# Optimization experiments

Measured on AMD Instinct MI355X. Metric: run time of the kernel, lower is better.

Reference implementation:

```python
import jax, jax.numpy as jnp
import numpy as np

N = 8192       # batch size
BIT = 32       # hash code length
NCLASS = 100   # number of classes
ALPHA = 0.1    # config['alpha'] (quantization weight)
BEITA = 1.0    # config['beita'] (classification weight)
GAMMA = 0.1    # config['gamma'] (balancing weight)
P = 2          # config['p']


def setup_inputs() -> dict:
    key = jax.random.key(0)
    k1, k2, k3 = jax.random.split(key, 3)
    u = jax.random.normal(k1, (N, BIT), dtype=jnp.float32)
    Y = jax.random.normal(k2, (N, NCLASS), dtype=jnp.float32)
    labels = jax.random.randint(k3, (N,), 0, NCLASS)
    y = jax.nn.one_hot(labels, NCLASS, dtype=jnp.float32)  # one-hot targets
    return {"u": u, "Y": Y, "y": y}


def _hash_loss(u, y):
    n = u.shape[0]
    theta = (u @ u.T) * 0.5                       # [N, N]
    sim = (y @ y.T > 0).astype(u.dtype)           # [N, N] pairwise same-class
    # log(1 + exp(theta)) - Sim * theta  (logaddexp = stable same math)
    pair = jnp.logaddexp(0.0, theta) - sim * theta
    mask_pos = sim > 0
    s1 = sim.sum() - n                            # positives minus diagonal
    s0 = n * n - sim.sum()                        # negatives
    s0 = jnp.where(s0 == 0, 1.0, s0)
    s1 = jnp.where(s1 == 0, 1.0, s1)
    s = s0 + s1
    scale = jnp.where(mask_pos, s / s1, s / s0)
    pair = pair * scale
    # original subtracts diag of the *detached* rescaled matrix
    pair = pair - jax.lax.stop_gradient(jnp.diag(jnp.diag(pair)))
    count = n * (n - 1) / 2
    return pair.sum() / 2.0 / count


def reference(u, Y, y):
    likelihood_loss = _hash_loss(u, y)
    # CrossEntropyLoss with soft (one-hot float) targets
    logp = jax.nn.log_softmax(Y, axis=-1)
    classification_loss = -(y * logp).sum(axis=-1).mean()
    m = u.mean(axis=1)
    if P == 1:
        quantization_loss = ALPHA * jnp.abs(m).mean()
    else:
        quantization_loss = ALPHA * (m ** 2).mean()
    b = jnp.sign(u)
    balancing_loss = GAMMA * ((u - b) ** 2).mean()
    return likelihood_loss + BEITA * classification_loss + quantization_loss + balancing_loss
```

## Files before the change

### kernel.cpp

```cpp
#include <hip/hip_runtime.h>
#include <math.h>
#include <type_traits>

#define N 8192
#define BIT 32
#define NCLASS 100
#define ALPHA 0.1
#define BEITA 1.0
#define GAMMA 0.1

#define BT 128
#define NT (N / BT)
#define NPAIRBLK (NT * (NT + 1) / 2)
#define NPREP (N / 8)

typedef __attribute__((ext_vector_type(8))) short s16x8;
typedef __attribute__((ext_vector_type(4))) float f32x4;

static __device__ __forceinline__ unsigned short f2bf(float f) {
    unsigned int x = __float_as_uint(f);
    x += 0x7fff + ((x >> 16) & 1);
    return (unsigned short)(x >> 16);
}


__global__ __launch_bounds__(256) void prep_kernel(
    const float* __restrict__ u, const float* __restrict__ Y, const float* __restrict__ y,
    int* __restrict__ labels, double* __restrict__ Pc, double* __restrict__ Pm,
    double* __restrict__ Pb)
{
    const int t = threadIdx.x;
    const int lane = t & 63;
    const int w = t >> 6;
    const int row0 = blockIdx.x * 8;

    float wcls = 0.f;
    #pragma unroll
    for (int rr = 0; rr < 2; ++rr) {
        const int r = row0 + w * 2 + rr;
        const float* Yp = Y + (size_t)r * NCLASS;
        const float* yp = y + (size_t)r * NCLASS;
        const bool has2 = lane < (NCLASS - 64);
        float Y0 = Yp[lane];
        float Y1 = has2 ? Yp[64 + lane] : -1e30f;
        float y0 = yp[lane];
        float y1 = has2 ? yp[64 + lane] : 0.f;
        float m = fmaxf(Y0, Y1);
        #pragma unroll
        for (int o = 32; o; o >>= 1) m = fmaxf(m, __shfl_xor(m, o, 64));
        float e  = __expf(Y0 - m) + (has2 ? __expf(Y1 - m) : 0.f);
        float tg = y0 * Y0 + (has2 ? y1 * Y1 : 0.f);
        #pragma unroll
        for (int o = 32; o; o >>= 1) { e += __shfl_xor(e, o, 64); tg += __shfl_xor(tg, o, 64); }
        unsigned long long b0 = __ballot(y0 > 0.5f);
        unsigned long long b1 = __ballot(has2 && (y1 > 0.5f));
        if (lane == 0) {
            int lbl = b0 ? (__ffsll((long long)b0) - 1) : (64 + __ffsll((long long)b1) - 1);
            labels[r] = lbl;
            wcls += m + __logf(e) - tg;
        }
    }

    const float x = u[(size_t)row0 * BIT + t];
    float bb = (x > 0.f) ? 1.f : ((x < 0.f) ? -1.f : 0.f);
    float d = x - bb;
    float bal = d * d;
    float rs = x;
    #pragma unroll
    for (int o = 1; o < 32; o <<= 1) rs += __shfl_xor(rs, o, 64);
    float mrow = rs * (1.f / BIT);
    float m2 = ((t & 31) == 0) ? mrow * mrow : 0.f;
    #pragma unroll
    for (int o = 32; o; o >>= 1) { m2 += __shfl_down(m2, o, 64); bal += __shfl_down(bal, o, 64); }

    __shared__ double red[4][3];
    if (lane == 0) { red[w][0] = (double)wcls; red[w][1] = (double)m2; red[w][2] = (double)bal; }
    __syncthreads();
    if (t == 0) {
        Pc[blockIdx.x] = red[0][0] + red[1][0] + red[2][0] + red[3][0];
        Pm[blockIdx.x] = red[0][1] + red[1][1] + red[2][1] + red[3][1];
        Pb[blockIdx.x] = red[0][2] + red[1][2] + red[2][2] + red[3][2];
    }
}

__global__ __launch_bounds__(256, 4) void pair_kernel(
    const float* __restrict__ u, const int* __restrict__ labels,
    double* __restrict__ Ppos, double* __restrict__ Pneg)
{
    const int b = blockIdx.x;
    int ti = (int)(((float)(2 * NT + 1) - sqrtf((float)((2 * NT + 1) * (2 * NT + 1) - 8 * b))) * 0.5f);
    int S = ti * (2 * NT - ti + 1) / 2;
    if (S > b) { --ti; S = ti * (2 * NT - ti + 1) / 2; }
    else { int S2 = (ti + 1) * (2 * NT - ti) / 2; if (S2 <= b) { ++ti; S = S2; } }
    const int tj = ti + (b - S);
    const int i0 = ti * BT, j0 = tj * BT;

    __shared__ __align__(16) unsigned short Us[4][256][8];
    __shared__ int Ls[256];
    __shared__ float wredp[4], wredn[4];

    const int t = threadIdx.x;

    {
        const int g = (t < BT) ? (i0 + t) : (j0 + t - BT);
        const float4* p = (const float4*)(u + (size_t)g * BIT);
        #pragma unroll
        for (int c = 0; c < 4; ++c) {
            float4 v0 = p[2 * c], v1 = p[2 * c + 1];
            s16x8 fr;
            fr[0] = (short)f2bf(v0.x); fr[1] = (short)f2bf(v0.y);
            fr[2] = (short)f2bf(v0.z); fr[3] = (short)f2bf(v0.w);
            fr[4] = (short)f2bf(v1.x); fr[5] = (short)f2bf(v1.y);
            fr[6] = (short)f2bf(v1.z); fr[7] = (short)f2bf(v1.w);
            *(s16x8*)&Us[c][t][0] = fr;
        }
        Ls[t] = labels[g];
    }
    __syncthreads();

    const int lane = t & 63;
    const int w = t >> 6;
    const int wy = w >> 1, wx = w & 1;
    const int quad = lane >> 4, lr = lane & 15;

    s16x8 av[4], bv[4];
    #pragma unroll
    for (int x = 0; x < 4; ++x) {
        av[x] = *(const s16x8*)&Us[quad][wy * 64 + x * 16 + lr][0];
        bv[x] = *(const s16x8*)&Us[quad][128 + wx * 64 + x * 16 + lr][0];
    }
    int lbv[4], lav[16];
    #pragma unroll
    for (int c = 0; c < 4; ++c) lbv[c] = Ls[128 + wx * 64 + c * 16 + lr];
    #pragma unroll
    for (int a = 0; a < 4; ++a)
        #pragma unroll
        for (int r = 0; r < 4; ++r) lav[a * 4 + r] = Ls[wy * 64 + a * 16 + quad * 4 + r];

    float sp0 = 0.f, sp1 = 0.f, sn0 = 0.f, sn1 = 0.f;
    auto run = [&](auto DIAGC) {
        constexpr bool DIAG = decltype(DIAGC)::value;
        f32x4 accf[4][4];
        #pragma unroll
        for (int a = 0; a < 4; ++a)
            #pragma unroll
            for (int c = 0; c < 4; ++c)
                accf[a][c] = __builtin_amdgcn_mfma_f32_16x16x32_bf16(
                    av[a], bv[c], (f32x4){0.f, 0.f, 0.f, 0.f}, 0, 0, 0);

        #pragma unroll
        for (int a = 0; a < 4; ++a) {
            #pragma unroll
            for (int c = 0; c < 4; ++c) {
                const int lb = lbv[c];
                #pragma unroll
                for (int r = 0; r < 4; ++r) {
                    const float v = accf[a][c][r];
                    const bool sim = (lav[a * 4 + r] == lb);
                    float hv = 0.5f * v;
                    float e  = exp2f(-1.44269504f * fabsf(hv));
                    float lt = 0.69314718f * __log2f(1.f + e);
                    float tp = fmaxf(-hv, 0.f) + lt;
                    float tn = tp + hv;
                    if (DIAG) {
                        const int lrow = wy * 64 + a * 16 + quad * 4 + r;
                        const int lcol = wx * 64 + c * 16 + lr;
                        const bool keep = lcol > lrow;
                        tp = keep ? tp : 0.f;
                        tn = keep ? tn : 0.f;
                    }
                    float up = sim ? tp : 0.f;
                    float un = sim ? 0.f : tn;
                    if (r & 1) { sp1 += up; sn1 += un; }
                    else       { sp0 += up; sn0 += un; }
                }
            }
        }
    };
    if (ti == tj) run(std::integral_constant<bool, true>{});
    else          run(std::integral_constant<bool, false>{});

    float sp = sp0 + sp1, sn = sn0 + sn1;
    #pragma unroll
    for (int o = 32; o; o >>= 1) { sp += __shfl_down(sp, o, 64); sn += __shfl_down(sn, o, 64); }
    if (lane == 0) { wredp[w] = sp; wredn[w] = sn; }
    __syncthreads();
    if (t == 0) {
        Ppos[b] = (double)(wredp[0] + wredp[1] + wredp[2] + wredp[3]);
        Pneg[b] = (double)(wredn[0] + wredn[1] + wredn[2] + wredn[3]);
    }
}

__global__ __launch_bounds__(256) void fin_kernel(
    const int* __restrict__ labels, const double* __restrict__ Ppos,
    const double* __restrict__ Pneg, const double* __restrict__ Pc,
    const double* __restrict__ Pm, const double* __restrict__ Pb, float* __restrict__ out)
{
    __shared__ int h[128];
    __shared__ double red[4][5];
    __shared__ double scd[2];
    const int t = threadIdx.x;
    const int lane = t & 63;
    const int w = t >> 6;

    if (t < 128) h[t] = 0;
    __syncthreads();
    #pragma unroll
    for (int k = 0; k < 32; ++k) atomicAdd(&h[labels[t + k * 256]], 1);
    __syncthreads();

    if (w == 0) {
        long long c0 = (lane < NCLASS) ? h[lane] : 0;
        long long c1 = (lane + 64 < NCLASS) ? h[lane + 64] : 0;
        long long ss = c0 * c0 + c1 * c1;
        #pragma unroll
        for (int o = 32; o; o >>= 1) ss += __shfl_xor(ss, o, 64);
        if (lane == 0) {
            double s1 = (double)ss - (double)N;
            double s0 = (double)N * (double)N - (double)ss;
            if (s0 == 0.0) s0 = 1.0;
            if (s1 == 0.0) s1 = 1.0;
            double s = s0 + s1;
            scd[0] = s / s1;
            scd[1] = s / s0;
        }
    }

    double p0 = 0, p1 = 0, cc = 0, mm = 0, bb = 0;
    for (int i = t; i < NPAIRBLK; i += 256) { p0 += Ppos[i]; p1 += Pneg[i]; }
    for (int i = t; i < NPREP; i += 256)    { cc += Pc[i]; mm += Pm[i]; bb += Pb[i]; }
    #pragma unroll
    for (int o = 32; o; o >>= 1) {
        p0 += __shfl_down(p0, o, 64); p1 += __shfl_down(p1, o, 64);
        cc += __shfl_down(cc, o, 64); mm += __shfl_down(mm, o, 64);
        bb += __shfl_down(bb, o, 64);
    }
    if (lane == 0) { red[w][0] = p0; red[w][1] = p1; red[w][2] = cc; red[w][3] = mm; red[w][4] = bb; }
    __syncthreads();
    if (t == 0) {
        double a_pos = red[0][0] + red[1][0] + red[2][0] + red[3][0];
        double a_neg = red[0][1] + red[1][1] + red[2][1] + red[3][1];
        double a_cls = red[0][2] + red[1][2] + red[2][2] + red[3][2];
        double a_m2  = red[0][3] + red[1][3] + red[2][3] + red[3][3];
        double a_bal = red[0][4] + red[1][4] + red[2][4] + red[3][4];
        double pairsum = scd[0] * a_pos + scd[1] * a_neg;
        double lik   = 2.0 * pairsum / ((double)N * (double)(N - 1));
        double cls   = a_cls / (double)N;
        double quant = ALPHA * (a_m2 / (double)N);
        double bal   = GAMMA * (a_bal / ((double)N * (double)BIT));
        out[0] = (float)(lik + BEITA * cls + quant + bal);
    }
}

extern "C" void kernel_launch(void* const* d_in, const int* in_sizes, int n_in,
                              void* d_out, int out_size, void* d_ws, size_t ws_size,
                              hipStream_t stream) {
    const float* u = (const float*)d_in[0];
    const float* Y = (const float*)d_in[1];
    const float* y = (const float*)d_in[2];
    float* out = (float*)d_out;

    char* ws = (char*)d_ws;
    int*    labels = (int*)(ws + 1024);
    double* Ppos   = (double*)(ws + 40960);
    double* Pneg   = (double*)(ws + 61440);
    double* Pc     = (double*)(ws + 81920);
    double* Pm     = (double*)(ws + 90112);
    double* Pb     = (double*)(ws + 98304);

    prep_kernel<<<NPREP, 256, 0, stream>>>(u, Y, y, labels, Pc, Pm, Pb);
    pair_kernel<<<NPAIRBLK, 256, 0, stream>>>(u, labels, Ppos, Pneg);
    fin_kernel<<<1, 256, 0, stream>>>(labels, Ppos, Pneg, Pc, Pm, Pb, out);
}
```

Before: 98.13 us.

## Precompute pre-scaled bf16 codes in prep and move softplus to base-2

The prep kernel now writes a bf16 copy of u pre-scaled by sqrt(0.5*log2 e) and 8-bit labels. The pair kernel then loads MFMA fragments straight from global memory, dropping the LDS staging, the per-block fp32-to-bf16 conversion and the block barrier. The softplus is computed in base 2 using raw exp2/log2 builtins, with the ln2 factor folded into the final scale constants. Folding the scale before bf16 rounding changes the rounding slightly, and loading 16-byte fragments uncoalesced from global memory relies on the cache.

Result: faster. 92.46 us (-5.8%).

```diff
diff --git a/kernel.cpp b/kernel.cpp
--- a/kernel.cpp
+++ b/kernel.cpp
@@ -14,8 +14,22 @@
 #define NPAIRBLK (NT * (NT + 1) / 2)
 #define NPREP (N / 8)
 
+#define SCALE_BF 0.84932181f
+#define LN2 0.6931471805599453
+
 typedef __attribute__((ext_vector_type(8))) short s16x8;
 typedef __attribute__((ext_vector_type(4))) float f32x4;
+
+#if __has_builtin(__builtin_amdgcn_exp2f)
+static __device__ __forceinline__ float fexp2(float x) { return __builtin_amdgcn_exp2f(x); }
+#else
+static __device__ __forceinline__ float fexp2(float x) { return exp2f(x); }
+#endif
+#if __has_builtin(__builtin_amdgcn_logf)
+static __device__ __forceinline__ float flog2(float x) { return __builtin_amdgcn_logf(x); }
+#else
+static __device__ __forceinline__ float flog2(float x) { return __log2f(x); }
+#endif
 
 static __device__ __forceinline__ unsigned short f2bf(float f) {
     unsigned int x = __float_as_uint(f);
@@ -26,8 +40,8 @@
 
 __global__ __launch_bounds__(256) void prep_kernel(
     const float* __restrict__ u, const float* __restrict__ Y, const float* __restrict__ y,
-    int* __restrict__ labels, double* __restrict__ Pc, double* __restrict__ Pm,
-    double* __restrict__ Pb)
+    unsigned char* __restrict__ lab8, unsigned short* __restrict__ ubf,
+    double* __restrict__ Pc, double* __restrict__ Pm, double* __restrict__ Pb)
 {
     const int t = threadIdx.x;
     const int lane = t & 63;
@@ -56,12 +70,14 @@
         unsigned long long b1 = __ballot(has2 && (y1 > 0.5f));
         if (lane == 0) {
             int lbl = b0 ? (__ffsll((long long)b0) - 1) : (64 + __ffsll((long long)b1) - 1);
-            labels[r] = lbl;
+            lab8[r] = (unsigned char)lbl;
             wcls += m + __logf(e) - tg;
         }
     }
 
-    const float x = u[(size_t)row0 * BIT + t];
+    const size_t uidx = (size_t)row0 * BIT + t;
+    const float x = u[uidx];
+    ubf[uidx] = f2bf(x * SCALE_BF);
     float bb = (x > 0.f) ? 1.f : ((x < 0.f) ? -1.f : 0.f);
     float d = x - bb;
     float bal = d * d;
@@ -84,7 +100,7 @@
 }
 
 __global__ __launch_bounds__(256, 4) void pair_kernel(
-    const float* __restrict__ u, const int* __restrict__ labels,
+    const unsigned short* __restrict__ ubf, const unsigned char* __restrict__ lab8,
     double* __restrict__ Ppos, double* __restrict__ Pneg)
 {
     const int b = blockIdx.x;
@@ -95,82 +111,57 @@
     const int tj = ti + (b - S);
     const int i0 = ti * BT, j0 = tj * BT;
 
-    __shared__ __align__(16) unsigned short Us[4][256][8];
-    __shared__ int Ls[256];
-    __shared__ float wredp[4], wredn[4];
-
     const int t = threadIdx.x;
-
-    {
-        const int g = (t < BT) ? (i0 + t) : (j0 + t - BT);
-        const float4* p = (const float4*)(u + (size_t)g * BIT);
-        #pragma unroll
-        for (int c = 0; c < 4; ++c) {
-            float4 v0 = p[2 * c], v1 = p[2 * c + 1];
-            s16x8 fr;
-            fr[0] = (short)f2bf(v0.x); fr[1] = (short)f2bf(v0.y);
-            fr[2] = (short)f2bf(v0.z); fr[3] = (short)f2bf(v0.w);
-            fr[4] = (short)f2bf(v1.x); fr[5] = (short)f2bf(v1.y);
-            fr[6] = (short)f2bf(v1.z); fr[7] = (short)f2bf(v1.w);
-            *(s16x8*)&Us[c][t][0] = fr;
-        }
-        Ls[t] = labels[g];
-    }
-    __syncthreads();
-
     const int lane = t & 63;
     const int w = t >> 6;
     const int wy = w >> 1, wx = w & 1;
     const int quad = lane >> 4, lr = lane & 15;
+    const int ar = i0 + wy * 64;
+    const int br = j0 + wx * 64;
 
     s16x8 av[4], bv[4];
     #pragma unroll
     for (int x = 0; x < 4; ++x) {
-        av[x] = *(const s16x8*)&Us[quad][wy * 64 + x * 16 + lr][0];
-        bv[x] = *(const s16x8*)&Us[quad][128 + wx * 64 + x * 16 + lr][0];
-    }
-    int lbv[4], lav[16];
-    #pragma unroll
-    for (int c = 0; c < 4; ++c) lbv[c] = Ls[128 + wx * 64 + c * 16 + lr];
-    #pragma unroll
-    for (int a = 0; a < 4; ++a)
-        #pragma unroll
-        for (int r = 0; r < 4; ++r) lav[a * 4 + r] = Ls[wy * 64 + a * 16 + quad * 4 + r];
+        av[x] = *(const s16x8*)(ubf + (size_t)(ar + x * 16 + lr) * BIT + quad * 8);
+        bv[x] = *(const s16x8*)(ubf + (size_t)(br + x * 16 + lr) * BIT + quad * 8);
+    }
+    int lavp[4], lbv[4];
+    #pragma unroll
+    for (int a = 0; a < 4; ++a) lavp[a] = *(const int*)(lab8 + ar + a * 16 + quad * 4);
+    #pragma unroll
+    for (int c = 0; c < 4; ++c) lbv[c] = (int)lab8[br + c * 16 + lr];
 
     float sp0 = 0.f, sp1 = 0.f, sn0 = 0.f, sn1 = 0.f;
     auto run = [&](auto DIAGC) {
         constexpr bool DIAG = decltype(DIAGC)::value;
-        f32x4 accf[4][4];
-        #pragma unroll
-        for (int a = 0; a < 4; ++a)
+        #pragma unroll
+        for (int a = 0; a < 4; ++a) {
+            f32x4 acc[4];
             #pragma unroll
             for (int c = 0; c < 4; ++c)
-                accf[a][c] = __builtin_amdgcn_mfma_f32_16x16x32_bf16(
+                acc[c] = __builtin_amdgcn_mfma_f32_16x16x32_bf16(
                     av[a], bv[c], (f32x4){0.f, 0.f, 0.f, 0.f}, 0, 0, 0);
 
-        #pragma unroll
-        for (int a = 0; a < 4; ++a) {
             #pragma unroll
-            for (int c = 0; c < 4; ++c) {
-                const int lb = lbv[c];
+            for (int r = 0; r < 4; ++r) {
+                const int la = (lavp[a] >> (r * 8)) & 0xff;
+                const int lrow = wy * 64 + a * 16 + quad * 4 + r;
                 #pragma unroll
-                for (int r = 0; r < 4; ++r) {
-                    const float v = accf[a][c][r];
-                    const bool sim = (lav[a * 4 + r] == lb);
-                    float hv = 0.5f * v;
-                    float e  = exp2f(-1.44269504f * fabsf(hv));
-                    float lt = 0.69314718f * __log2f(1.f + e);
-                    float tp = fmaxf(-hv, 0.f) + lt;
-                    float tn = tp + hv;
+                for (int c = 0; c < 4; ++c) {
+                    const float tv = acc[c][r];
+                    float e  = fexp2(-fabsf(tv));
+                    float l  = flog2(1.f + e);
+                    float sl = fmaxf(tv, 0.f) + l;
+                    float d  = sl - tv;
+                    const bool sim = (la == lbv[c]);
+                    float up = sim ? d : 0.f;
+                    float un = sim ? 0.f : sl;
                     if (DIAG) {
-                        const int lrow = wy * 64 + a * 16 + quad * 4 + r;
                         const int lcol = wx * 64 + c * 16 + lr;
                         const bool keep = lcol > lrow;
-                        tp = keep ? tp : 0.f;
-                        tn = keep ? tn : 0.f;
+                        up = keep ? up : 0.f;
+                        un = keep ? un : 0.f;
                     }
-                    float up = sim ? tp : 0.f;
-                    float un = sim ? 0.f : tn;
                     if (r & 1) { sp1 += up; sn1 += un; }
                     else       { sp0 += up; sn0 += un; }
                 }
@@ -183,6 +174,7 @@
     float sp = sp0 + sp1, sn = sn0 + sn1;
     #pragma unroll
     for (int o = 32; o; o >>= 1) { sp += __shfl_down(sp, o, 64); sn += __shfl_down(sn, o, 64); }
+    __shared__ float wredp[4], wredn[4];
     if (lane == 0) { wredp[w] = sp; wredn[w] = sn; }
     __syncthreads();
     if (t == 0) {
@@ -192,7 +184,7 @@
 }
 
 __global__ __launch_bounds__(256) void fin_kernel(
-    const int* __restrict__ labels, const double* __restrict__ Ppos,
+    const unsigned char* __restrict__ lab8, const double* __restrict__ Ppos,
     const double* __restrict__ Pneg, const double* __restrict__ Pc,
     const double* __restrict__ Pm, const double* __restrict__ Pb, float* __restrict__ out)
 {
@@ -206,7 +198,7 @@
     if (t < 128) h[t] = 0;
     __syncthreads();
     #pragma unroll
-    for (int k = 0; k < 32; ++k) atomicAdd(&h[labels[t + k * 256]], 1);
+    for (int k = 0; k < 32; ++k) atomicAdd(&h[lab8[t + k * 256]], 1);
     __syncthreads();
 
     if (w == 0) {
@@ -221,8 +213,8 @@
             if (s0 == 0.0) s0 = 1.0;
             if (s1 == 0.0) s1 = 1.0;
             double s = s0 + s1;
-            scd[0] = s / s1;
-            scd[1] = s / s0;
+            scd[0] = (s / s1) * LN2;
+            scd[1] = (s / s0) * LN2;
         }
     }
 
@@ -261,14 +253,15 @@
     float* out = (float*)d_out;
 
     char* ws = (char*)d_ws;
-    int*    labels = (int*)(ws + 1024);
-    double* Ppos   = (double*)(ws + 40960);
-    double* Pneg   = (double*)(ws + 61440);
-    double* Pc     = (double*)(ws + 81920);
-    double* Pm     = (double*)(ws + 90112);
-    double* Pb     = (double*)(ws + 98304);
-
-    prep_kernel<<<NPREP, 256, 0, stream>>>(u, Y, y, labels, Pc, Pm, Pb);
-    pair_kernel<<<NPAIRBLK, 256, 0, stream>>>(u, labels, Ppos, Pneg);
-    fin_kernel<<<1, 256, 0, stream>>>(labels, Ppos, Pneg, Pc, Pm, Pb, out);
-}
+    unsigned char*  lab8 = (unsigned char*)(ws + 1024);
+    unsigned short* ubf  = (unsigned short*)(ws + 16384);
+    double* Ppos = (double*)(ws + 557056);
+    double* Pneg = (double*)(ws + 581632);
+    double* Pc   = (double*)(ws + 606208);
+    double* Pm   = (double*)(ws + 614400);
+    double* Pb   = (double*)(ws + 622592);
+
+    prep_kernel<<<NPREP, 256, 0, stream>>>(u, Y, y, lab8, ubf, Pc, Pm, Pb);
+    pair_kernel<<<NPAIRBLK, 256, 0, stream>>>(ubf, lab8, Ppos, Pneg);
+    fin_kernel<<<1, 256, 0, stream>>>(lab8, Ppos, Pneg, Pc, Pm, Pb, out);
+}
```
